# Kernel tuning notes

Measured on AMD Instinct MI355X. Metric: run time of the kernel, lower is better.

## Reference

```python
import jax, jax.numpy as jnp
import numpy as np

N_NODES = 65536
N_EDGES = 524288
FEAT_DIM = 512
EMBED_DIM = 512


def setup_inputs() -> dict:
    key = jax.random.key(0)
    k1, k2, k3, k4, k5 = jax.random.split(key, 5)
    x = jax.random.normal(k1, (N_NODES, FEAT_DIM), dtype=jnp.float32)
    # xavier_uniform for (embed_dim, feat_dim)
    limit = float(np.sqrt(6.0 / (EMBED_DIM + FEAT_DIM)))
    weight = jax.random.uniform(k2, (EMBED_DIM, FEAT_DIM), dtype=jnp.float32,
                                minval=-limit, maxval=limit)
    row = jax.random.randint(k3, (N_EDGES,), 0, N_NODES, dtype=jnp.int64)
    col = jax.random.randint(k4, (N_EDGES,), 0, N_NODES, dtype=jnp.int64)
    vals = jax.random.uniform(k5, (N_EDGES,), dtype=jnp.float32)
    return {"x": x, "weight": weight, "row": row, "col": col, "vals": vals}


def reference(x, weight, row, col, vals):
    # Fused GEMM + SpMM: out = adj @ (x @ weight.T)
    h = jnp.einsum('nf,ef->ne', x, weight)            # [N, embed_dim] dense GEMM
    msgs = vals[:, None] * h[col]                     # [E, embed_dim] gather + scale
    out = jax.ops.segment_sum(msgs, row, num_segments=N_NODES)  # SpMM scatter-add
    return out
```

## Files before the change

kernel.cpp:

```cpp
#include <hip/hip_runtime.h>
#include <stdint.h>


#define N_NODES 65536
#define N_EDGES 524288
#define FEAT    512
#define EMB     512
#define CAP     64

typedef short  short8  __attribute__((ext_vector_type(8)));
typedef float  floatx4 __attribute__((ext_vector_type(4)));
typedef unsigned int uintx2 __attribute__((ext_vector_type(2)));

__device__ __forceinline__ unsigned short f2bf(float f) {
    unsigned int u = __float_as_uint(f);
    u += 0x7FFFu + ((u >> 16) & 1u);
    return (unsigned short)(u >> 16);
}
__device__ __forceinline__ float bf2f_lo(unsigned int u){ return __uint_as_float(u << 16); }
__device__ __forceinline__ float bf2f_hi(unsigned int u){ return __uint_as_float(u & 0xffff0000u); }

typedef __attribute__((address_space(1))) const void* gas_vp;
typedef __attribute__((address_space(3))) void*       las_vp;
#define GLDS16(g, l) __builtin_amdgcn_global_load_lds((gas_vp)(const void*)(g), (las_vp)(void*)(l), 16, 0, 0)

__global__ __launch_bounds__(256)
void prep(const float* __restrict__ w, unsigned short* __restrict__ wb,
          int* __restrict__ cnt)
{
    size_t i = (size_t)blockIdx.x * 256 + threadIdx.x;
    size_t j = i * 8;
    floatx4 a = *(const floatx4*)&w[j];
    floatx4 b = *(const floatx4*)&w[j + 4];
    ushort4 lo, hi;
    lo.x = f2bf(a.x); lo.y = f2bf(a.y); lo.z = f2bf(a.z); lo.w = f2bf(a.w);
    hi.x = f2bf(b.x); hi.y = f2bf(b.y); hi.z = f2bf(b.z); hi.w = f2bf(b.w);
    *(ushort4*)&wb[j]     = lo;
    *(ushort4*)&wb[j + 4] = hi;
    int2 z; z.x = 0; z.y = 0;
    *(int2*)&cnt[i * 2] = z;
}

__global__ __launch_bounds__(512, 4)
void gemm_fill(const float* __restrict__ x, const unsigned short* __restrict__ wb,
               unsigned short* __restrict__ h,
               const int* __restrict__ row, const int* __restrict__ col,
               const float* __restrict__ vals,
               int* __restrict__ cnt, uintx2* __restrict__ ebuf)
{
    __shared__ unsigned short As[64 * 64];
    __shared__ unsigned short Bs[512 * 64];

    if (blockIdx.x & 1) {
        int e = (blockIdx.x >> 1) * 512 + threadIdx.x;
        int   r = __builtin_nontemporal_load(&row[e]);
        int   c = __builtin_nontemporal_load(&col[e]);
        float v = __builtin_nontemporal_load(&vals[e]);
        int slot = atomicAdd(&cnt[r], 1);
        if (slot < CAP) {
            uintx2 ev; ev.x = (unsigned)c; ev.y = __float_as_uint(v);
            ebuf[r * CAP + slot] = ev;
        }
        return;
    }

    const int gid  = blockIdx.x >> 1;
    const int t    = threadIdx.x;
    const int lane = t & 63;
    const int wave = t >> 6;
    const int l15  = lane & 15;
    const int lq   = lane >> 4;

    const int m0 = gid * 64;

    const int r8 = t >> 3;
    const int c8 = t & 7;

    floatx4 acc[4][4];
    #pragma unroll
    for (int i = 0; i < 4; i++)
        #pragma unroll
        for (int j = 0; j < 4; j++) acc[i][j] = (floatx4){0.f, 0.f, 0.f, 0.f};

    float4 xa, xb_;
    {
        const float* px = &x[(size_t)(m0 + r8) * FEAT + c8 * 8];
        xa  = *(const float4*)px;
        xb_ = *(const float4*)(px + 4);
    }

    for (int kb = 0; kb < FEAT; kb += 64) {
        #pragma unroll
        for (int p = 0; p < 8; p++) {
            int brow = p * 64 + r8;
            int lc   = c8 ^ (r8 & 7);
            GLDS16(&wb[brow * FEAT + kb + lc * 8], &Bs[brow * 64 + c8 * 8]);
        }
        {
            short8 v;
            v[0] = (short)f2bf(xa.x);  v[1] = (short)f2bf(xa.y);
            v[2] = (short)f2bf(xa.z);  v[3] = (short)f2bf(xa.w);
            v[4] = (short)f2bf(xb_.x); v[5] = (short)f2bf(xb_.y);
            v[6] = (short)f2bf(xb_.z); v[7] = (short)f2bf(xb_.w);
            *(short8*)&As[r8 * 64 + (c8 ^ (r8 & 7)) * 8] = v;
        }
        __syncthreads();

        if (kb + 64 < FEAT) {
            const float* px = &x[(size_t)(m0 + r8) * FEAT + (kb + 64) + c8 * 8];
            xa  = *(const float4*)px;
            xb_ = *(const float4*)(px + 4);
        }

        #pragma unroll
        for (int kk = 0; kk < 2; kk++) {
            short8 af[4], bfr[4];
            #pragma unroll
            for (int mt = 0; mt < 4; mt++) {
                int r  = mt * 16 + l15;
                int pc = (kk * 4 + lq) ^ (r & 7);
                af[mt] = *(const short8*)&As[r * 64 + pc * 8];
            }
            #pragma unroll
            for (int nt = 0; nt < 4; nt++) {
                int r  = wave * 64 + nt * 16 + l15;
                int pc = (kk * 4 + lq) ^ (r & 7);
                bfr[nt] = *(const short8*)&Bs[r * 64 + pc * 8];
            }
            #pragma unroll
            for (int mt = 0; mt < 4; mt++)
                #pragma unroll
                for (int nt = 0; nt < 4; nt++)
                    acc[mt][nt] = __builtin_amdgcn_mfma_f32_16x16x32_bf16(
                        af[mt], bfr[nt], acc[mt][nt], 0, 0, 0);
        }
        __syncthreads();
    }

    #pragma unroll
    for (int mt = 0; mt < 4; mt++)
        #pragma unroll
        for (int nt = 0; nt < 4; nt++)
            #pragma unroll
            for (int r = 0; r < 4; r++) {
                int orow = m0 + mt * 16 + lq * 4 + r;
                int ocol = wave * 64 + nt * 16 + l15;
                h[(size_t)orow * EMB + ocol] = f2bf(acc[mt][nt][r]);
            }
}

#define BM 128
#define BN 64
#define LDA 72

__global__ __launch_bounds__(256)
void gemm_f32(const float* __restrict__ x, const float* __restrict__ w,
              unsigned short* __restrict__ h)
{
    __shared__ unsigned short As2[BM][LDA];
    __shared__ unsigned short Bs2[BN][LDA];

    const int t = threadIdx.x, lane = t & 63, wave = t >> 6;
    const int wm = wave >> 1, wn = wave & 1;
    const int l15 = lane & 15, lq = lane >> 4;
    const int xcd = blockIdx.x & 7;
    const int loc = blockIdx.x >> 3;
    const int m0 = (xcd * 64 + (loc >> 3)) * BM;
    const int n0 = (loc & 7) * BN;

    floatx4 acc[4][2];
    #pragma unroll
    for (int i = 0; i < 4; i++)
        #pragma unroll
        for (int j = 0; j < 2; j++) acc[i][j] = (floatx4){0.f, 0.f, 0.f, 0.f};

    for (int kb = 0; kb < FEAT; kb += 64) {
        #pragma unroll
        for (int p = 0; p < 8; p++) {
            int idx = p * 256 + t, r = idx >> 4, cv = (idx & 15) << 2;
            float4 v = *(const float4*)&x[(m0 + r) * FEAT + kb + cv];
            ushort4 b4 = {f2bf(v.x), f2bf(v.y), f2bf(v.z), f2bf(v.w)};
            *(ushort4*)&As2[r][cv] = b4;
        }
        #pragma unroll
        for (int p = 0; p < 4; p++) {
            int idx = p * 256 + t, r = idx >> 4, cv = (idx & 15) << 2;
            float4 v = *(const float4*)&w[(n0 + r) * FEAT + kb + cv];
            ushort4 b4 = {f2bf(v.x), f2bf(v.y), f2bf(v.z), f2bf(v.w)};
            *(ushort4*)&Bs2[r][cv] = b4;
        }
        __syncthreads();
        #pragma unroll
        for (int kk = 0; kk < 2; kk++) {
            short8 af[4], bf[2];
            #pragma unroll
            for (int mt = 0; mt < 4; mt++)
                af[mt] = *(const short8*)&As2[wm * 64 + mt * 16 + l15][kk * 32 + lq * 8];
            #pragma unroll
            for (int nt = 0; nt < 2; nt++)
                bf[nt] = *(const short8*)&Bs2[wn * 32 + nt * 16 + l15][kk * 32 + lq * 8];
            #pragma unroll
            for (int mt = 0; mt < 4; mt++)
                #pragma unroll
                for (int nt = 0; nt < 2; nt++)
                    acc[mt][nt] = __builtin_amdgcn_mfma_f32_16x16x32_bf16(
                        af[mt], bf[nt], acc[mt][nt], 0, 0, 0);
        }
        __syncthreads();
    }
    #pragma unroll
    for (int mt = 0; mt < 4; mt++)
        #pragma unroll
        for (int nt = 0; nt < 2; nt++)
            #pragma unroll
            for (int r = 0; r < 4; r++) {
                int orow = m0 + wm * 64 + mt * 16 + lq * 4 + r;
                int ocol = n0 + wn * 32 + nt * 16 + l15;
                h[orow * EMB + ocol] = f2bf(acc[mt][nt][r]);
            }
}

__global__ __launch_bounds__(256)
void fill_edges(const int* __restrict__ row, const int* __restrict__ col,
                const float* __restrict__ vals, int* __restrict__ cnt,
                uintx2* __restrict__ ebuf)
{
    int e = blockIdx.x * 256 + threadIdx.x;
    int   r = __builtin_nontemporal_load(&row[e]);
    int   c = __builtin_nontemporal_load(&col[e]);
    float v = __builtin_nontemporal_load(&vals[e]);
    int slot = atomicAdd(&cnt[r], 1);
    if (slot < CAP) {
        uintx2 ev; ev.x = (unsigned)c; ev.y = __float_as_uint(v);
        ebuf[r * CAP + slot] = ev;
    }
}

__global__ __launch_bounds__(256)
void rowsum(const unsigned short* __restrict__ h, const int* __restrict__ cnt,
            const uintx2* __restrict__ ebuf, float* __restrict__ out)
{
    const int r    = blockIdx.x * 4 + (threadIdx.x >> 6);
    const int lane = threadIdx.x & 63;
    int deg = cnt[r];
    if (deg > CAP) deg = CAP;
    const int base = r * CAP;

    int   c_l = 0;
    float v_l = 0.f;
    if (lane < deg) {
        uintx2 ev = ebuf[base + lane];
        c_l = (int)ev.x;
        v_l = __uint_as_float(ev.y);
    }

    float acc[8] = {0.f,0.f,0.f,0.f,0.f,0.f,0.f,0.f};
    for (int i0 = 0; i0 < deg; i0 += 8) {
        uint4 hv[8]; float vv[8];
        int nn = deg - i0; if (nn > 8) nn = 8;
        #pragma unroll
        for (int j = 0; j < 8; j++) {
            if (j < nn) {
                int c = __shfl(c_l, i0 + j, 64);
                vv[j] = __shfl(v_l, i0 + j, 64);
                hv[j] = *(const uint4*)&h[(size_t)c * EMB + lane * 8];
            }
        }
        #pragma unroll
        for (int j = 0; j < 8; j++) {
            if (j < nn) {
                float v = vv[j];
                acc[0] += v * bf2f_lo(hv[j].x); acc[1] += v * bf2f_hi(hv[j].x);
                acc[2] += v * bf2f_lo(hv[j].y); acc[3] += v * bf2f_hi(hv[j].y);
                acc[4] += v * bf2f_lo(hv[j].z); acc[5] += v * bf2f_hi(hv[j].z);
                acc[6] += v * bf2f_lo(hv[j].w); acc[7] += v * bf2f_hi(hv[j].w);
            }
        }
    }
    floatx4* o = (floatx4*)&out[(size_t)r * EMB + lane * 8];
    floatx4 o0; o0.x = acc[0]; o0.y = acc[1]; o0.z = acc[2]; o0.w = acc[3];
    floatx4 o1; o1.x = acc[4]; o1.y = acc[5]; o1.z = acc[6]; o1.w = acc[7];
    __builtin_nontemporal_store(o0, o);
    __builtin_nontemporal_store(o1, o + 1);
}

__global__ __launch_bounds__(128)
void scatter_atomic(const int* __restrict__ row, const int* __restrict__ col,
                    const float* __restrict__ vals, const unsigned short* __restrict__ h,
                    float* __restrict__ out)
{
    int e = blockIdx.x;
    int r = row[e], c = col[e];
    float v = vals[e];
    int f = threadIdx.x * 4;
    uint2 hv = *(const uint2*)&h[c * EMB + f];
    float* o = &out[r * EMB + f];
    atomicAdd(o + 0, v * bf2f_lo(hv.x));
    atomicAdd(o + 1, v * bf2f_hi(hv.x));
    atomicAdd(o + 2, v * bf2f_lo(hv.y));
    atomicAdd(o + 3, v * bf2f_hi(hv.y));
}

extern "C" void kernel_launch(void* const* d_in, const int* in_sizes, int n_in,
                              void* d_out, int out_size, void* d_ws, size_t ws_size,
                              hipStream_t stream) {
    const float* x    = (const float*)d_in[0];
    const float* w    = (const float*)d_in[1];
    const int*   row  = (const int*)d_in[2];
    const int*   col  = (const int*)d_in[3];
    const float* vals = (const float*)d_in[4];
    float* out = (float*)d_out;
    char* ws = (char*)d_ws;

    const size_t SZ_WB  = (size_t)EMB * FEAT * 2;
    const size_t SZ_H   = (size_t)N_NODES * EMB * 2;
    const size_t SZ_CNT = (size_t)N_NODES * 4;
    const size_t SZ_E   = (size_t)N_NODES * CAP * 8;
    const size_t NEED_FAST = SZ_WB + SZ_H + SZ_CNT + SZ_E;
    const size_t NEED_BIN  = SZ_H + SZ_CNT + SZ_E;

    if (ws_size >= NEED_FAST) {
        unsigned short* wb = (unsigned short*)ws;
        unsigned short* h  = (unsigned short*)(ws + SZ_WB);
        int*    cnt  = (int*)(ws + SZ_WB + SZ_H);
        uintx2* ebuf = (uintx2*)(ws + SZ_WB + SZ_H + SZ_CNT);

        prep<<<dim3(128), dim3(256), 0, stream>>>(w, wb, cnt);
        gemm_fill<<<dim3(2048), dim3(512), 0, stream>>>(x, wb, h, row, col, vals, cnt, ebuf);
        rowsum<<<dim3(N_NODES / 4), dim3(256), 0, stream>>>(h, cnt, ebuf, out);
    } else if (ws_size >= NEED_BIN) {
        unsigned short* h = (unsigned short*)ws;
        int*    cnt  = (int*)(ws + SZ_H);
        uintx2* ebuf = (uintx2*)(ws + SZ_H + SZ_CNT);

        gemm_f32<<<dim3(4096), dim3(256), 0, stream>>>(x, w, h);
        (void)hipMemsetAsync(cnt, 0, SZ_CNT, stream);
        fill_edges<<<dim3(N_EDGES / 256), dim3(256), 0, stream>>>(row, col, vals, cnt, ebuf);
        rowsum<<<dim3(N_NODES / 4), dim3(256), 0, stream>>>(h, cnt, ebuf, out);
    } else {
        unsigned short* h = (unsigned short*)ws;
        gemm_f32<<<dim3(4096), dim3(256), 0, stream>>>(x, w, h);
        (void)hipMemsetAsync(out, 0, (size_t)out_size * sizeof(float), stream);
        scatter_atomic<<<dim3(N_EDGES), dim3(128), 0, stream>>>(row, col, vals, h, out);
    }
}
```

Before: 410.7 us.

## Split edge fill from GEMM and retile GEMM to 64x256 with XCD swizzle

Edge binning moves out of the fused GEMM kernel into its own fill_edges launch. The GEMM is rewritten as gemm_fused with 64x256 output tiles and 40KB of shared memory, allowing up to 8 resident waves per SIMD via launch bounds. A block-index swizzle keeps the two N-halves of the same row tile on the same XCD so the x rows can be reused from L2. The aim is higher GEMM occupancy and an end to mixing divergent block types in one grid. The cost is an extra kernel launch and x being read twice per row tile.

```diff
diff --git a/kernel.cpp b/kernel.cpp
--- a/kernel.cpp
+++ b/kernel.cpp
@@ -41,185 +41,6 @@
     *(int2*)&cnt[i * 2] = z;
 }
 
-__global__ __launch_bounds__(512, 4)
-void gemm_fill(const float* __restrict__ x, const unsigned short* __restrict__ wb,
-               unsigned short* __restrict__ h,
-               const int* __restrict__ row, const int* __restrict__ col,
-               const float* __restrict__ vals,
-               int* __restrict__ cnt, uintx2* __restrict__ ebuf)
-{
-    __shared__ unsigned short As[64 * 64];
-    __shared__ unsigned short Bs[512 * 64];
-
-    if (blockIdx.x & 1) {
-        int e = (blockIdx.x >> 1) * 512 + threadIdx.x;
-        int   r = __builtin_nontemporal_load(&row[e]);
-        int   c = __builtin_nontemporal_load(&col[e]);
-        float v = __builtin_nontemporal_load(&vals[e]);
-        int slot = atomicAdd(&cnt[r], 1);
-        if (slot < CAP) {
-            uintx2 ev; ev.x = (unsigned)c; ev.y = __float_as_uint(v);
-            ebuf[r * CAP + slot] = ev;
-        }
-        return;
-    }
-
-    const int gid  = blockIdx.x >> 1;
-    const int t    = threadIdx.x;
-    const int lane = t & 63;
-    const int wave = t >> 6;
-    const int l15  = lane & 15;
-    const int lq   = lane >> 4;
-
-    const int m0 = gid * 64;
-
-    const int r8 = t >> 3;
-    const int c8 = t & 7;
-
-    floatx4 acc[4][4];
-    #pragma unroll
-    for (int i = 0; i < 4; i++)
-        #pragma unroll
-        for (int j = 0; j < 4; j++) acc[i][j] = (floatx4){0.f, 0.f, 0.f, 0.f};
-
-    float4 xa, xb_;
-    {
-        const float* px = &x[(size_t)(m0 + r8) * FEAT + c8 * 8];
-        xa  = *(const float4*)px;
-        xb_ = *(const float4*)(px + 4);
-    }
-
-    for (int kb = 0; kb < FEAT; kb += 64) {
-        #pragma unroll
-        for (int p = 0; p < 8; p++) {
-            int brow = p * 64 + r8;
-            int lc   = c8 ^ (r8 & 7);
-            GLDS16(&wb[brow * FEAT + kb + lc * 8], &Bs[brow * 64 + c8 * 8]);
-        }
-        {
-            short8 v;
-            v[0] = (short)f2bf(xa.x);  v[1] = (short)f2bf(xa.y);
-            v[2] = (short)f2bf(xa.z);  v[3] = (short)f2bf(xa.w);
-            v[4] = (short)f2bf(xb_.x); v[5] = (short)f2bf(xb_.y);
-            v[6] = (short)f2bf(xb_.z); v[7] = (short)f2bf(xb_.w);
-            *(short8*)&As[r8 * 64 + (c8 ^ (r8 & 7)) * 8] = v;
-        }
-        __syncthreads();
-
-        if (kb + 64 < FEAT) {
-            const float* px = &x[(size_t)(m0 + r8) * FEAT + (kb + 64) + c8 * 8];
-            xa  = *(const float4*)px;
-            xb_ = *(const float4*)(px + 4);
-        }
-
-        #pragma unroll
-        for (int kk = 0; kk < 2; kk++) {
-            short8 af[4], bfr[4];
-            #pragma unroll
-            for (int mt = 0; mt < 4; mt++) {
-                int r  = mt * 16 + l15;
-                int pc = (kk * 4 + lq) ^ (r & 7);
-                af[mt] = *(const short8*)&As[r * 64 + pc * 8];
-            }
-            #pragma unroll
-            for (int nt = 0; nt < 4; nt++) {
-                int r  = wave * 64 + nt * 16 + l15;
-                int pc = (kk * 4 + lq) ^ (r & 7);
-                bfr[nt] = *(const short8*)&Bs[r * 64 + pc * 8];
-            }
-            #pragma unroll
-            for (int mt = 0; mt < 4; mt++)
-                #pragma unroll
-                for (int nt = 0; nt < 4; nt++)
-                    acc[mt][nt] = __builtin_amdgcn_mfma_f32_16x16x32_bf16(
-                        af[mt], bfr[nt], acc[mt][nt], 0, 0, 0);
-        }
-        __syncthreads();
-    }
-
-    #pragma unroll
-    for (int mt = 0; mt < 4; mt++)
-        #pragma unroll
-        for (int nt = 0; nt < 4; nt++)
-            #pragma unroll
-            for (int r = 0; r < 4; r++) {
-                int orow = m0 + mt * 16 + lq * 4 + r;
-                int ocol = wave * 64 + nt * 16 + l15;
-                h[(size_t)orow * EMB + ocol] = f2bf(acc[mt][nt][r]);
-            }
-}
-
-#define BM 128
-#define BN 64
-#define LDA 72
-
-__global__ __launch_bounds__(256)
-void gemm_f32(const float* __restrict__ x, const float* __restrict__ w,
-              unsigned short* __restrict__ h)
-{
-    __shared__ unsigned short As2[BM][LDA];
-    __shared__ unsigned short Bs2[BN][LDA];
-
-    const int t = threadIdx.x, lane = t & 63, wave = t >> 6;
-    const int wm = wave >> 1, wn = wave & 1;
-    const int l15 = lane & 15, lq = lane >> 4;
-    const int xcd = blockIdx.x & 7;
-    const int loc = blockIdx.x >> 3;
-    const int m0 = (xcd * 64 + (loc >> 3)) * BM;
-    const int n0 = (loc & 7) * BN;
-
-    floatx4 acc[4][2];
-    #pragma unroll
-    for (int i = 0; i < 4; i++)
-        #pragma unroll
-        for (int j = 0; j < 2; j++) acc[i][j] = (floatx4){0.f, 0.f, 0.f, 0.f};
-
-    for (int kb = 0; kb < FEAT; kb += 64) {
-        #pragma unroll
-        for (int p = 0; p < 8; p++) {
-            int idx = p * 256 + t, r = idx >> 4, cv = (idx & 15) << 2;
-            float4 v = *(const float4*)&x[(m0 + r) * FEAT + kb + cv];
-            ushort4 b4 = {f2bf(v.x), f2bf(v.y), f2bf(v.z), f2bf(v.w)};
-            *(ushort4*)&As2[r][cv] = b4;
-        }
-        #pragma unroll
-        for (int p = 0; p < 4; p++) {
-            int idx = p * 256 + t, r = idx >> 4, cv = (idx & 15) << 2;
-            float4 v = *(const float4*)&w[(n0 + r) * FEAT + kb + cv];
-            ushort4 b4 = {f2bf(v.x), f2bf(v.y), f2bf(v.z), f2bf(v.w)};
-            *(ushort4*)&Bs2[r][cv] = b4;
-        }
-        __syncthreads();
-        #pragma unroll
-        for (int kk = 0; kk < 2; kk++) {
-            short8 af[4], bf[2];
-            #pragma unroll
-            for (int mt = 0; mt < 4; mt++)
-                af[mt] = *(const short8*)&As2[wm * 64 + mt * 16 + l15][kk * 32 + lq * 8];
-            #pragma unroll
-            for (int nt = 0; nt < 2; nt++)
-                bf[nt] = *(const short8*)&Bs2[wn * 32 + nt * 16 + l15][kk * 32 + lq * 8];
-            #pragma unroll
-            for (int mt = 0; mt < 4; mt++)
-                #pragma unroll
-                for (int nt = 0; nt < 2; nt++)
-                    acc[mt][nt] = __builtin_amdgcn_mfma_f32_16x16x32_bf16(
-                        af[mt], bf[nt], acc[mt][nt], 0, 0, 0);
-        }
-        __syncthreads();
-    }
-    #pragma unroll
-    for (int mt = 0; mt < 4; mt++)
-        #pragma unroll
-        for (int nt = 0; nt < 2; nt++)
-            #pragma unroll
-            for (int r = 0; r < 4; r++) {
-                int orow = m0 + wm * 64 + mt * 16 + lq * 4 + r;
-                int ocol = n0 + wn * 32 + nt * 16 + l15;
-                h[orow * EMB + ocol] = f2bf(acc[mt][nt][r]);
-            }
-}
-
 __global__ __launch_bounds__(256)
 void fill_edges(const int* __restrict__ row, const int* __restrict__ col,
                 const float* __restrict__ vals, int* __restrict__ cnt,
@@ -234,6 +55,171 @@
         uintx2 ev; ev.x = (unsigned)c; ev.y = __float_as_uint(v);
         ebuf[r * CAP + slot] = ev;
     }
+}
+
+__global__ __launch_bounds__(512, 8)
+void gemm_fused(const float* __restrict__ x, const unsigned short* __restrict__ wb,
+                unsigned short* __restrict__ h)
+{
+    __shared__ unsigned short As[64 * 64];
+    __shared__ unsigned short Bs[256 * 64];
+
+    const int bid = blockIdx.x;
+    const int lid = (bid & 7) * 256 + (bid >> 3);
+    const int m0  = (lid >> 1) * 64;
+    const int n0  = (lid & 1) * 256;
+
+    const int t    = threadIdx.x;
+    const int lane = t & 63;
+    const int wave = t >> 6;
+    const int l15  = lane & 15;
+    const int lq   = lane >> 4;
+
+    const int r8 = t >> 3;
+    const int c8 = t & 7;
+
+    floatx4 acc[4][2];
+    #pragma unroll
+    for (int i = 0; i < 4; i++)
+        #pragma unroll
+        for (int j = 0; j < 2; j++) acc[i][j] = (floatx4){0.f, 0.f, 0.f, 0.f};
+
+    float4 xa, xb_;
+    {
+        const float* px = &x[(size_t)(m0 + r8) * FEAT + c8 * 8];
+        xa  = *(const float4*)px;
+        xb_ = *(const float4*)(px + 4);
+    }
+
+    for (int kb = 0; kb < FEAT; kb += 64) {
+        #pragma unroll
+        for (int p = 0; p < 4; p++) {
+            int brow = p * 64 + r8;
+            int lc   = c8 ^ (r8 & 7);
+            GLDS16(&wb[(size_t)(n0 + brow) * FEAT + kb + lc * 8], &Bs[brow * 64 + c8 * 8]);
+        }
+        {
+            short8 v;
+            v[0] = (short)f2bf(xa.x);  v[1] = (short)f2bf(xa.y);
+            v[2] = (short)f2bf(xa.z);  v[3] = (short)f2bf(xa.w);
+            v[4] = (short)f2bf(xb_.x); v[5] = (short)f2bf(xb_.y);
+            v[6] = (short)f2bf(xb_.z); v[7] = (short)f2bf(xb_.w);
+            *(short8*)&As[r8 * 64 + (c8 ^ (r8 & 7)) * 8] = v;
+        }
+        __syncthreads();
+
+        if (kb + 64 < FEAT) {
+            const float* px = &x[(size_t)(m0 + r8) * FEAT + (kb + 64) + c8 * 8];
+            xa  = *(const float4*)px;
+            xb_ = *(const float4*)(px + 4);
+        }
+
+        #pragma unroll
+        for (int kk = 0; kk < 2; kk++) {
+            short8 af[4], bfr[2];
+            #pragma unroll
+            for (int mt = 0; mt < 4; mt++) {
+                int r  = mt * 16 + l15;
+                int pc = (kk * 4 + lq) ^ (r & 7);
+                af[mt] = *(const short8*)&As[r * 64 + pc * 8];
+            }
+            #pragma unroll
+            for (int nt = 0; nt < 2; nt++) {
+                int r  = wave * 32 + nt * 16 + l15;
+                int pc = (kk * 4 + lq) ^ (r & 7);
+                bfr[nt] = *(const short8*)&Bs[r * 64 + pc * 8];
+            }
+            #pragma unroll
+            for (int mt = 0; mt < 4; mt++)
+                #pragma unroll
+                for (int nt = 0; nt < 2; nt++)
+                    acc[mt][nt] = __builtin_amdgcn_mfma_f32_16x16x32_bf16(
+                        af[mt], bfr[nt], acc[mt][nt], 0, 0, 0);
+        }
+        __syncthreads();
+    }
+
+    #pragma unroll
+    for (int mt = 0; mt < 4; mt++)
+        #pragma unroll
+        for (int nt = 0; nt < 2; nt++)
+            #pragma unroll
+            for (int r = 0; r < 4; r++) {
+                int orow = m0 + mt * 16 + lq * 4 + r;
+                int ocol = n0 + wave * 32 + nt * 16 + l15;
+                h[(size_t)orow * EMB + ocol] = f2bf(acc[mt][nt][r]);
+            }
+}
+
+#define BM 128
+#define BN 64
+#define LDA 72
+
+__global__ __launch_bounds__(256)
+void gemm_f32(const float* __restrict__ x, const float* __restrict__ w,
+              unsigned short* __restrict__ h)
+{
+    __shared__ unsigned short As2[BM][LDA];
+    __shared__ unsigned short Bs2[BN][LDA];
+
+    const int t = threadIdx.x, lane = t & 63, wave = t >> 6;
+    const int wm = wave >> 1, wn = wave & 1;
+    const int l15 = lane & 15, lq = lane >> 4;
+    const int xcd = blockIdx.x & 7;
+    const int loc = blockIdx.x >> 3;
+    const int m0 = (xcd * 64 + (loc >> 3)) * BM;
+    const int n0 = (loc & 7) * BN;
+
+    floatx4 acc[4][2];
+    #pragma unroll
+    for (int i = 0; i < 4; i++)
+        #pragma unroll
+        for (int j = 0; j < 2; j++) acc[i][j] = (floatx4){0.f, 0.f, 0.f, 0.f};
+
+    for (int kb = 0; kb < FEAT; kb += 64) {
+        #pragma unroll
+        for (int p = 0; p < 8; p++) {
+            int idx = p * 256 + t, r = idx >> 4, cv = (idx & 15) << 2;
+            float4 v = *(const float4*)&x[(m0 + r) * FEAT + kb + cv];
+            ushort4 b4 = {f2bf(v.x), f2bf(v.y), f2bf(v.z), f2bf(v.w)};
+            *(ushort4*)&As2[r][cv] = b4;
+        }
+        #pragma unroll
+        for (int p = 0; p < 4; p++) {
+            int idx = p * 256 + t, r = idx >> 4, cv = (idx & 15) << 2;
+            float4 v = *(const float4*)&w[(n0 + r) * FEAT + kb + cv];
+            ushort4 b4 = {f2bf(v.x), f2bf(v.y), f2bf(v.z), f2bf(v.w)};
+            *(ushort4*)&Bs2[r][cv] = b4;
+        }
+        __syncthreads();
+        #pragma unroll
+        for (int kk = 0; kk < 2; kk++) {
+            short8 af[4], bf[2];
+            #pragma unroll
+            for (int mt = 0; mt < 4; mt++)
+                af[mt] = *(const short8*)&As2[wm * 64 + mt * 16 + l15][kk * 32 + lq * 8];
+            #pragma unroll
+            for (int nt = 0; nt < 2; nt++)
+                bf[nt] = *(const short8*)&Bs2[wn * 32 + nt * 16 + l15][kk * 32 + lq * 8];
+            #pragma unroll
+            for (int mt = 0; mt < 4; mt++)
+                #pragma unroll
+                for (int nt = 0; nt < 2; nt++)
+                    acc[mt][nt] = __builtin_amdgcn_mfma_f32_16x16x32_bf16(
+                        af[mt], bf[nt], acc[mt][nt], 0, 0, 0);
+        }
+        __syncthreads();
+    }
+    #pragma unroll
+    for (int mt = 0; mt < 4; mt++)
+        #pragma unroll
+        for (int nt = 0; nt < 2; nt++)
+            #pragma unroll
+            for (int r = 0; r < 4; r++) {
+                int orow = m0 + wm * 64 + mt * 16 + lq * 4 + r;
+                int ocol = n0 + wn * 32 + nt * 16 + l15;
+                h[orow * EMB + ocol] = f2bf(acc[mt][nt][r]);
+            }
 }
 
 __global__ __launch_bounds__(256)
@@ -326,7 +312,8 @@
         uintx2* ebuf = (uintx2*)(ws + SZ_WB + SZ_H + SZ_CNT);
 
         prep<<<dim3(128), dim3(256), 0, stream>>>(w, wb, cnt);
-        gemm_fill<<<dim3(2048), dim3(512), 0, stream>>>(x, wb, h, row, col, vals, cnt, ebuf);
+        fill_edges<<<dim3(N_EDGES / 256), dim3(256), 0, stream>>>(row, col, vals, cnt, ebuf);
+        gemm_fused<<<dim3(2048), dim3(512), 0, stream>>>(x, wb, h);
         rowsum<<<dim3(N_NODES / 4), dim3(256), 0, stream>>>(h, cnt, ebuf, out);
     } else if (ws_size >= NEED_BIN) {
         unsigned short* h = (unsigned short*)ws;
```

Result: slower. 422.5 us (+2.9%).
